# Kernel tuning notes

Measured on AMD Instinct MI355X. Metric: run time of the kernel, lower is better.

Reference implementation:

```python
import jax, jax.numpy as jnp
import numpy as np

B, S, E, H = 8, 4096, 1024, 1024


def log_g(x):
    # log(relu(x)+0.5) for x>=0, -softplus(-x) for x<0
    return jnp.where(x >= 0, jnp.log(jax.nn.relu(x) + 0.5), -jax.nn.softplus(-x))


def parallel_scan_log(log_coeffs, log_values):
    # log_coeffs: (B,S,H); log_values: (B,S+1,H)
    a_star = jnp.cumsum(log_coeffs, axis=1)
    a_star = jnp.pad(a_star, ((0, 0), (1, 0), (0, 0)))  # (B,S+1,H)
    log_h0_plus_b_star = jax.lax.cumlogsumexp(log_values - a_star, axis=1)
    log_h = a_star + log_h0_plus_b_star
    return jnp.exp(log_h)[:, 1:]  # (B,S,H)


def setup_inputs() -> dict:
    key = jax.random.key(0)
    ks = jax.random.split(key, 8)
    scale = 1.0 / np.sqrt(E)
    return {
        "x": jax.random.normal(ks[0], (B, S, E), dtype=jnp.float32),
        "h_0": jax.random.uniform(ks[1], (B, 1, H), dtype=jnp.float32),
        "Wz": jax.random.normal(ks[2], (E, H), dtype=jnp.float32) * scale,
        "bz": jnp.zeros((H,), dtype=jnp.float32),
        "Wh": jax.random.normal(ks[3], (E, H), dtype=jnp.float32) * scale,
        "bh": jnp.zeros((H,), dtype=jnp.float32),
        "Wo": jax.random.normal(ks[4], (H, E), dtype=jnp.float32) * scale,
        "bo": jnp.zeros((E,), dtype=jnp.float32),
    }


def reference(x, h_0, Wz, bz, Wh, bh, Wo, bo):
    k = jnp.einsum("bse,eh->bsh", x, Wz) + bz
    log_z = -jax.nn.softplus(-k)
    log_coeffs = -jax.nn.softplus(k)
    log_h_0 = log_g(h_0)                                       # (B,1,H)
    log_tilde_h = log_g(jnp.einsum("bse,eh->bsh", x, Wh) + bh)  # (B,S,H)
    log_values = jnp.concatenate([log_h_0, log_z + log_tilde_h], axis=1)
    h = parallel_scan_log(log_coeffs, log_values)               # (B,S,H)
    out = jnp.einsum("bsh,he->bse", h, Wo) + bo
    return out, h[:, -1:, :]
```

## Files before the change

kernel.cpp:

```cpp
#include <hip/hip_runtime.h>
#include <hip/hip_bf16.h>
#include <cstdint>
#include <cstddef>

static constexpr int Bb   = 8;
static constexpr int Ss   = 4096;
static constexpr int Ee   = 1024;
static constexpr int Hh   = 1024;
static constexpr int Mtot = Bb * Ss;
static constexpr int NCH  = 32;
static constexpr int SCH  = Ss / NCH;

using f32x4 = __attribute__((ext_vector_type(4))) float;
using s16x8 = __attribute__((ext_vector_type(8))) short;
using u16x8 = __attribute__((ext_vector_type(8))) unsigned short;

__device__ __forceinline__ uint16_t f2bf(float f) {
  union { float f; uint32_t u; } c; c.f = f;
  uint32_t u = c.u;
  return (uint16_t)((u + 0x7FFFu + ((u >> 16) & 1u)) >> 16);
}
__device__ __forceinline__ float bf2f(uint32_t lo16) {
  union { uint32_t u; float f; } c; c.u = lo16 << 16;
  return c.f;
}

__global__ void cast_x_kernel(const float* __restrict__ x,
                              uint16_t* __restrict__ xb, int n) {
  int stride = gridDim.x * blockDim.x * 8;
  for (int i = (blockIdx.x * blockDim.x + threadIdx.x) * 8; i < n; i += stride) {
    const float4* p = (const float4*)(x + i);
    float4 v0 = p[0];
    float4 v1 = p[1];
    u16x8 r;
    r[0] = f2bf(v0.x); r[1] = f2bf(v0.y); r[2] = f2bf(v0.z); r[3] = f2bf(v0.w);
    r[4] = f2bf(v1.x); r[5] = f2bf(v1.y); r[6] = f2bf(v1.z); r[7] = f2bf(v1.w);
    *(u16x8*)(xb + i) = r;
  }
}

__global__ void wprep_kernel(const float* __restrict__ Wz,
                             const float* __restrict__ Wh,
                             const float* __restrict__ Wo,
                             uint16_t* __restrict__ Wzt,
                             uint16_t* __restrict__ Wht,
                             uint16_t* __restrict__ Wot) {
  __shared__ float tile[64][65];
  const float* src = (blockIdx.z == 0) ? Wz : (blockIdx.z == 1) ? Wh : Wo;
  uint16_t*    dst = (blockIdx.z == 0) ? Wzt : (blockIdx.z == 1) ? Wht : Wot;
  int k0 = blockIdx.x * 64, n0 = blockIdx.y * 64;
  int t = threadIdx.x;
  int c = t & 63, r0 = t >> 6;
  #pragma unroll
  for (int i = 0; i < 16; i++) {
    int r = r0 + i * 4;
    tile[r][c] = src[(size_t)(k0 + r) * 1024 + n0 + c];
  }
  __syncthreads();
  int k = t & 63, nn0 = t >> 6;
  #pragma unroll
  for (int i = 0; i < 16; i++) {
    int n = nn0 + i * 4;
    dst[(size_t)(n0 + n) * 1024 + k0 + k] = f2bf(tile[k][n]);
  }
}

template <bool DUAL>
__global__ __launch_bounds__(256)
void gemm_kernel(const uint16_t* __restrict__ A,
                 const uint16_t* __restrict__ Bt0,
                 const uint16_t* __restrict__ Bt1,
                 const float* __restrict__ bias0,
                 const float* __restrict__ bias1,
                 uint32_t* __restrict__ cv_out,
                 float* __restrict__ out,
                 int M, int N, int K) {
  constexpr int LDT = 40;
  __shared__ uint16_t As[128 * LDT];
  __shared__ uint16_t Bs0[64 * LDT];
  __shared__ uint16_t Bs1[DUAL ? 64 * LDT : 8];

  const int t = threadIdx.x;
  const int lane = t & 63, wid = t >> 6;
  const int wr = wid >> 1, wc = wid & 1;
  const int lr = lane & 15, kg = lane >> 4;
  const int m_base = blockIdx.x * 128;
  const int n_base = blockIdx.y * 64;

  f32x4 zero = {0.f, 0.f, 0.f, 0.f};
  f32x4 acc0[4][2];
  f32x4 acc1[DUAL ? 4 : 1][2];
  #pragma unroll
  for (int i = 0; i < 4; i++)
    #pragma unroll
    for (int j = 0; j < 2; j++) acc0[i][j] = zero;
  if constexpr (DUAL) {
    #pragma unroll
    for (int i = 0; i < 4; i++)
      #pragma unroll
      for (int j = 0; j < 2; j++) acc1[i][j] = zero;
  }

  for (int k0 = 0; k0 < K; k0 += 32) {
    #pragma unroll
    for (int i = 0; i < 2; i++) {
      int s = t + i * 256;
      int row = s >> 2, c16 = s & 3;
      s16x8 v = *(const s16x8*)(A + (size_t)(m_base + row) * K + k0 + c16 * 8);
      *(s16x8*)(As + row * LDT + c16 * 8) = v;
    }
    {
      int row = t >> 2, c16 = t & 3;
      s16x8 v = *(const s16x8*)(Bt0 + (size_t)(n_base + row) * K + k0 + c16 * 8);
      *(s16x8*)(Bs0 + row * LDT + c16 * 8) = v;
      if constexpr (DUAL) {
        s16x8 v1 = *(const s16x8*)(Bt1 + (size_t)(n_base + row) * K + k0 + c16 * 8);
        *(s16x8*)(Bs1 + row * LDT + c16 * 8) = v1;
      }
    }
    __syncthreads();

    s16x8 af[4], bf0[2], bf1[2];
    #pragma unroll
    for (int mf = 0; mf < 4; mf++)
      af[mf] = *(const s16x8*)(As + (wr * 64 + mf * 16 + lr) * LDT + kg * 8);
    #pragma unroll
    for (int nf = 0; nf < 2; nf++) {
      bf0[nf] = *(const s16x8*)(Bs0 + (wc * 32 + nf * 16 + lr) * LDT + kg * 8);
      if constexpr (DUAL)
        bf1[nf] = *(const s16x8*)(Bs1 + (wc * 32 + nf * 16 + lr) * LDT + kg * 8);
    }
    #pragma unroll
    for (int mf = 0; mf < 4; mf++)
      #pragma unroll
      for (int nf = 0; nf < 2; nf++) {
        acc0[mf][nf] = __builtin_amdgcn_mfma_f32_16x16x32_bf16(
            af[mf], bf0[nf], acc0[mf][nf], 0, 0, 0);
        if constexpr (DUAL)
          acc1[mf][nf] = __builtin_amdgcn_mfma_f32_16x16x32_bf16(
              af[mf], bf1[nf], acc1[mf][nf], 0, 0, 0);
      }
    __syncthreads();
  }

  #pragma unroll
  for (int mf = 0; mf < 4; mf++) {
    #pragma unroll
    for (int nf = 0; nf < 2; nf++) {
      #pragma unroll
      for (int j = 0; j < 4; j++) {
        int row = m_base + wr * 64 + mf * 16 + kg * 4 + j;
        int col = n_base + wc * 32 + nf * 16 + lr;
        if constexpr (DUAL) {
          float kv = acc0[mf][nf][j] + bias0[col];
          float av = acc1[mf][nf][j] + bias1[col];
          float zf = 1.f / (1.f + __expf(-kv));
          float cf = 1.f / (1.f + __expf(kv));
          float gf = (av >= 0.f) ? (av + 0.5f)
                                 : (1.f / (1.f + __expf(-av)));
          float vf = zf * gf;
          cv_out[(size_t)row * N + col] =
              (uint32_t)f2bf(cf) | ((uint32_t)f2bf(vf) << 16);
        } else {
          out[(size_t)row * N + col] = acc0[mf][nf][j] + bias0[col];
        }
      }
    }
  }
  (void)Bt1; (void)bias1; (void)cv_out; (void)out;
}

__global__ void scan1_kernel(const uint32_t* __restrict__ cv,
                             float* __restrict__ Cc, float* __restrict__ Vc) {
  int h = blockIdx.x * 256 + threadIdx.x;
  int j = blockIdx.y, b = blockIdx.z;
  size_t base = ((size_t)b * Ss + (size_t)j * SCH) * Hh + h;
  float C = 1.f, V = 0.f;
  #pragma unroll 4
  for (int s = 0; s < SCH; s++) {
    uint32_t p = cv[base + (size_t)s * Hh];
    float c = bf2f(p & 0xFFFFu), v = bf2f(p >> 16);
    C *= c;
    V = fmaf(c, V, v);
  }
  size_t o = ((size_t)b * NCH + j) * Hh + h;
  Cc[o] = C;
  Vc[o] = V;
}

__global__ void scan2_kernel(const float* __restrict__ h0,
                             const float* __restrict__ Cc,
                             const float* __restrict__ Vc,
                             float* __restrict__ hinit,
                             float* __restrict__ hlast) {
  int idx = blockIdx.x * 256 + threadIdx.x;
  float x = h0[idx];
  float st = (x >= 0.f) ? (x + 0.5f) : (1.f / (1.f + __expf(-x)));
  int b = idx >> 10, h = idx & 1023;
  for (int j = 0; j < NCH; j++) {
    size_t o = ((size_t)b * NCH + j) * Hh + h;
    hinit[o] = st;
    st = fmaf(Cc[o], st, Vc[o]);
  }
  hlast[idx] = st;
}

__global__ void scan3_kernel(const uint32_t* __restrict__ cv,
                             const float* __restrict__ hinit,
                             uint16_t* __restrict__ hb) {
  int h = blockIdx.x * 256 + threadIdx.x;
  int j = blockIdx.y, b = blockIdx.z;
  size_t base = ((size_t)b * Ss + (size_t)j * SCH) * Hh + h;
  float st = hinit[((size_t)b * NCH + j) * Hh + h];
  #pragma unroll 4
  for (int s = 0; s < SCH; s++) {
    uint32_t p = cv[base + (size_t)s * Hh];
    st = fmaf(bf2f(p & 0xFFFFu), st, bf2f(p >> 16));
    hb[base + (size_t)s * Hh] = f2bf(st);
  }
}

extern "C" void kernel_launch(void* const* d_in, const int* in_sizes, int n_in,
                              void* d_out, int out_size, void* d_ws, size_t ws_size,
                              hipStream_t stream) {
  const float* x  = (const float*)d_in[0];
  const float* h0 = (const float*)d_in[1];
  const float* Wz = (const float*)d_in[2];
  const float* bz = (const float*)d_in[3];
  const float* Wh = (const float*)d_in[4];
  const float* bh = (const float*)d_in[5];
  const float* Wo = (const float*)d_in[6];
  const float* bo = (const float*)d_in[7];
  float* out = (float*)d_out;

  uint32_t* cv = (uint32_t*)d_out;

  char* p = (char*)d_ws;
  uint16_t* xb  = (uint16_t*)p; p += (size_t)Mtot * Ee * 2;
  uint16_t* Wzt = (uint16_t*)p; p += (size_t)Ee * Hh * 2;
  uint16_t* Wht = (uint16_t*)p; p += (size_t)Ee * Hh * 2;
  uint16_t* Wot = (uint16_t*)p; p += (size_t)Hh * Ee * 2;
  float* Cc     = (float*)p;    p += (size_t)Bb * NCH * Hh * 4;
  float* Vc     = (float*)p;    p += (size_t)Bb * NCH * Hh * 4;
  float* hinit  = (float*)p;    p += (size_t)Bb * NCH * Hh * 4;
  uint16_t* hb  = (uint16_t*)p; p += (size_t)Mtot * Hh * 2;

  hipLaunchKernelGGL(cast_x_kernel, dim3(2048), dim3(256), 0, stream,
                     x, xb, Mtot * Ee);
  hipLaunchKernelGGL(wprep_kernel, dim3(16, 16, 3), dim3(256), 0, stream,
                     Wz, Wh, Wo, Wzt, Wht, Wot);
  hipLaunchKernelGGL((gemm_kernel<true>), dim3(Mtot / 128, Hh / 64), dim3(256), 0,
                     stream, xb, Wzt, Wht, bz, bh, cv, (float*)nullptr,
                     Mtot, Hh, Ee);
  hipLaunchKernelGGL(scan1_kernel, dim3(Hh / 256, NCH, Bb), dim3(256), 0, stream,
                     cv, Cc, Vc);
  hipLaunchKernelGGL(scan2_kernel, dim3((Bb * Hh) / 256), dim3(256), 0, stream,
                     h0, Cc, Vc, hinit, out + (size_t)Mtot * Ee);
  hipLaunchKernelGGL(scan3_kernel, dim3(Hh / 256, NCH, Bb), dim3(256), 0, stream,
                     cv, hinit, hb);
  hipLaunchKernelGGL((gemm_kernel<false>), dim3(Mtot / 128, Ee / 64), dim3(256), 0,
                     stream, hb, Wot, (const uint16_t*)nullptr, bo,
                     (const float*)nullptr, (uint32_t*)nullptr, out,
                     Mtot, Ee, Hh);
}
```

Measured before the change: 661.1 us.

## Use direct global-to-LDS loads in GEMM and widen output GEMM tile

Replaces the register-staged global→LDS tile copies with the global_load_lds builtin (16 bytes per lane), so data goes straight into LDS without passing through VGPRs. The LDS padding is removed as a result, which may cause bank conflicts on the fragment reads. It also templates the N tile width and runs the output projection GEMM with 128-wide N tiles, raising reuse of the A tile at the cost of more accumulator registers.

```diff
diff --git a/kernel.cpp b/kernel.cpp
--- a/kernel.cpp
+++ b/kernel.cpp
@@ -24,6 +24,11 @@
   union { uint32_t u; float f; } c; c.u = lo16 << 16;
   return c.f;
 }
+
+#define GLOAD_LDS16(gp, lp)                                                  \
+  __builtin_amdgcn_global_load_lds(                                          \
+      (const __attribute__((address_space(1))) void*)(gp),                   \
+      (__attribute__((address_space(3))) void*)(lp), 16, 0, 0)
 
 __global__ void cast_x_kernel(const float* __restrict__ x,
                               uint16_t* __restrict__ xb, int n) {
@@ -65,7 +70,7 @@
   }
 }
 
-template <bool DUAL>
+template <bool DUAL, int NT>
 __global__ __launch_bounds__(256)
 void gemm_kernel(const uint16_t* __restrict__ A,
                  const uint16_t* __restrict__ Bt0,
@@ -75,70 +80,75 @@
                  uint32_t* __restrict__ cv_out,
                  float* __restrict__ out,
                  int M, int N, int K) {
-  constexpr int LDT = 40;
-  __shared__ uint16_t As[128 * LDT];
-  __shared__ uint16_t Bs0[64 * LDT];
-  __shared__ uint16_t Bs1[DUAL ? 64 * LDT : 8];
+  constexpr int NFR = NT / 32;
+  __shared__ __align__(16) uint16_t As[128 * 32];
+  __shared__ __align__(16) uint16_t Bs0[NT * 32];
+  __shared__ __align__(16) uint16_t Bs1[DUAL ? NT * 32 : 8];
 
   const int t = threadIdx.x;
   const int lane = t & 63, wid = t >> 6;
   const int wr = wid >> 1, wc = wid & 1;
   const int lr = lane & 15, kg = lane >> 4;
   const int m_base = blockIdx.x * 128;
-  const int n_base = blockIdx.y * 64;
+  const int n_base = blockIdx.y * NT;
+  const int wcN = wc * (NT / 2);
+
+  const int srow = lane >> 2;
+  const int scol = (lane & 3) * 8;
+  const uint16_t* pA  = A   + (size_t)(m_base + wid * 16 + srow) * K + scol;
+  const uint16_t* pB0 = Bt0 + (size_t)(n_base + wid * 16 + srow) * K + scol;
+  const uint16_t* pB1 =
+      DUAL ? (Bt1 + (size_t)(n_base + wid * 16 + srow) * K + scol) : nullptr;
+  char* lA  = (char*)As  + wid * 1024;
+  char* lB0 = (char*)Bs0 + wid * 1024;
+  char* lB1 = (char*)Bs1 + wid * 1024;
 
   f32x4 zero = {0.f, 0.f, 0.f, 0.f};
-  f32x4 acc0[4][2];
-  f32x4 acc1[DUAL ? 4 : 1][2];
+  f32x4 acc0[4][NFR];
+  f32x4 acc1[DUAL ? 4 : 1][NFR];
   #pragma unroll
   for (int i = 0; i < 4; i++)
     #pragma unroll
-    for (int j = 0; j < 2; j++) acc0[i][j] = zero;
+    for (int j = 0; j < NFR; j++) acc0[i][j] = zero;
   if constexpr (DUAL) {
     #pragma unroll
     for (int i = 0; i < 4; i++)
       #pragma unroll
-      for (int j = 0; j < 2; j++) acc1[i][j] = zero;
+      for (int j = 0; j < NFR; j++) acc1[i][j] = zero;
   }
 
   for (int k0 = 0; k0 < K; k0 += 32) {
-    #pragma unroll
-    for (int i = 0; i < 2; i++) {
-      int s = t + i * 256;
-      int row = s >> 2, c16 = s & 3;
-      s16x8 v = *(const s16x8*)(A + (size_t)(m_base + row) * K + k0 + c16 * 8);
-      *(s16x8*)(As + row * LDT + c16 * 8) = v;
-    }
-    {
-      int row = t >> 2, c16 = t & 3;
-      s16x8 v = *(const s16x8*)(Bt0 + (size_t)(n_base + row) * K + k0 + c16 * 8);
-      *(s16x8*)(Bs0 + row * LDT + c16 * 8) = v;
-      if constexpr (DUAL) {
-        s16x8 v1 = *(const s16x8*)(Bt1 + (size_t)(n_base + row) * K + k0 + c16 * 8);
-        *(s16x8*)(Bs1 + row * LDT + c16 * 8) = v1;
-      }
+    GLOAD_LDS16(pA + k0, lA);
+    GLOAD_LDS16(pA + (size_t)64 * K + k0, lA + 4096);
+    GLOAD_LDS16(pB0 + k0, lB0);
+    if constexpr (NT == 128)
+      GLOAD_LDS16(pB0 + (size_t)64 * K + k0, lB0 + 4096);
+    if constexpr (DUAL) {
+      GLOAD_LDS16(pB1 + k0, lB1);
+      if constexpr (NT == 128)
+        GLOAD_LDS16(pB1 + (size_t)64 * K + k0, lB1 + 4096);
     }
     __syncthreads();
 
-    s16x8 af[4], bf0[2], bf1[2];
+    s16x8 af[4], b0f[NFR], b1f[NFR];
     #pragma unroll
     for (int mf = 0; mf < 4; mf++)
-      af[mf] = *(const s16x8*)(As + (wr * 64 + mf * 16 + lr) * LDT + kg * 8);
-    #pragma unroll
-    for (int nf = 0; nf < 2; nf++) {
-      bf0[nf] = *(const s16x8*)(Bs0 + (wc * 32 + nf * 16 + lr) * LDT + kg * 8);
+      af[mf] = *(const s16x8*)(As + (wr * 64 + mf * 16 + lr) * 32 + kg * 8);
+    #pragma unroll
+    for (int nf = 0; nf < NFR; nf++) {
+      b0f[nf] = *(const s16x8*)(Bs0 + (wcN + nf * 16 + lr) * 32 + kg * 8);
       if constexpr (DUAL)
-        bf1[nf] = *(const s16x8*)(Bs1 + (wc * 32 + nf * 16 + lr) * LDT + kg * 8);
+        b1f[nf] = *(const s16x8*)(Bs1 + (wcN + nf * 16 + lr) * 32 + kg * 8);
     }
     #pragma unroll
     for (int mf = 0; mf < 4; mf++)
       #pragma unroll
-      for (int nf = 0; nf < 2; nf++) {
+      for (int nf = 0; nf < NFR; nf++) {
         acc0[mf][nf] = __builtin_amdgcn_mfma_f32_16x16x32_bf16(
-            af[mf], bf0[nf], acc0[mf][nf], 0, 0, 0);
+            af[mf], b0f[nf], acc0[mf][nf], 0, 0, 0);
         if constexpr (DUAL)
           acc1[mf][nf] = __builtin_amdgcn_mfma_f32_16x16x32_bf16(
-              af[mf], bf1[nf], acc1[mf][nf], 0, 0, 0);
+              af[mf], b1f[nf], acc1[mf][nf], 0, 0, 0);
       }
     __syncthreads();
   }
@@ -146,11 +156,11 @@
   #pragma unroll
   for (int mf = 0; mf < 4; mf++) {
     #pragma unroll
-    for (int nf = 0; nf < 2; nf++) {
+    for (int nf = 0; nf < NFR; nf++) {
       #pragma unroll
       for (int j = 0; j < 4; j++) {
         int row = m_base + wr * 64 + mf * 16 + kg * 4 + j;
-        int col = n_base + wc * 32 + nf * 16 + lr;
+        int col = n_base + wcN + nf * 16 + lr;
         if constexpr (DUAL) {
           float kv = acc0[mf][nf][j] + bias0[col];
           float av = acc1[mf][nf][j] + bias1[col];
@@ -167,7 +177,7 @@
       }
     }
   }
-  (void)Bt1; (void)bias1; (void)cv_out; (void)out;
+  (void)pB1; (void)bias1; (void)cv_out; (void)out;
 }
 
 __global__ void scan1_kernel(const uint32_t* __restrict__ cv,
@@ -249,17 +259,17 @@
                      x, xb, Mtot * Ee);
   hipLaunchKernelGGL(wprep_kernel, dim3(16, 16, 3), dim3(256), 0, stream,
                      Wz, Wh, Wo, Wzt, Wht, Wot);
-  hipLaunchKernelGGL((gemm_kernel<true>), dim3(Mtot / 128, Hh / 64), dim3(256), 0,
-                     stream, xb, Wzt, Wht, bz, bh, cv, (float*)nullptr,
-                     Mtot, Hh, Ee);
+  hipLaunchKernelGGL((gemm_kernel<true, 64>), dim3(Mtot / 128, Hh / 64),
+                     dim3(256), 0, stream, xb, Wzt, Wht, bz, bh, cv,
+                     (float*)nullptr, Mtot, Hh, Ee);
   hipLaunchKernelGGL(scan1_kernel, dim3(Hh / 256, NCH, Bb), dim3(256), 0, stream,
                      cv, Cc, Vc);
   hipLaunchKernelGGL(scan2_kernel, dim3((Bb * Hh) / 256), dim3(256), 0, stream,
                      h0, Cc, Vc, hinit, out + (size_t)Mtot * Ee);
   hipLaunchKernelGGL(scan3_kernel, dim3(Hh / 256, NCH, Bb), dim3(256), 0, stream,
                      cv, hinit, hb);
-  hipLaunchKernelGGL((gemm_kernel<false>), dim3(Mtot / 128, Ee / 64), dim3(256), 0,
-                     stream, hb, Wot, (const uint16_t*)nullptr, bo,
-                     (const float*)nullptr, (uint32_t*)nullptr, out,
+  hipLaunchKernelGGL((gemm_kernel<false, 128>), dim3(Mtot / 128, Ee / 128),
+                     dim3(256), 0, stream, hb, Wot, (const uint16_t*)nullptr,
+                     bo, (const float*)nullptr, (uint32_t*)nullptr, out,
                      Mtot, Ee, Hh);
 }
```

New measurement: 622.4 us. -5.8%, faster.
